# Optimization experiments

Measured on AMD Instinct MI355X. Metric: run time of the kernel, lower is better.

## Reference

```python
import jax, jax.numpy as jnp
import numpy as np

H = 356  # CHAR_EMBED_DIM (100) + ELMO_EMBED_DIM (256)
CHAR_VOCAB = 96
CHAR_DIM = 100
N_FILT = 100
KW = 5
N_CTX = 8192
N_Q = 1024
W_CHARS = 16


def setup_inputs() -> dict:
    key = jax.random.key(0)
    ks = iter(jax.random.split(key, 32))
    s = 0.05
    inp = {}
    inp['ctx_char_ids'] = jax.random.randint(next(ks), (N_CTX, W_CHARS), 0, CHAR_VOCAB, dtype=jnp.int32)
    inp['q_char_ids'] = jax.random.randint(next(ks), (N_Q, W_CHARS), 0, CHAR_VOCAB, dtype=jnp.int32)
    inp['ctx_elmo'] = jax.random.normal(next(ks), (N_CTX, 256), jnp.float32)
    inp['q_elmo'] = jax.random.normal(next(ks), (N_Q, 256), jnp.float32)
    inp['char_emb'] = jax.random.normal(next(ks), (CHAR_VOCAB, CHAR_DIM), jnp.float32)
    inp['conv_w'] = jax.random.normal(next(ks), (N_FILT, CHAR_DIM, KW), jnp.float32) * s
    inp['conv_b'] = jax.random.normal(next(ks), (N_FILT,), jnp.float32) * s
    # Highway: 2 layers of plain + gate Linear(356 -> 356)
    inp['hw_pw'] = jax.random.normal(next(ks), (2, H, H), jnp.float32) * s
    inp['hw_pb'] = jax.random.normal(next(ks), (2, H), jnp.float32) * s
    inp['hw_gw'] = jax.random.normal(next(ks), (2, H, H), jnp.float32) * s
    inp['hw_gb'] = jax.random.normal(next(ks), (2, H), jnp.float32) * s
    # BiLSTM layer 0: input 356; layer 1: input 712. dims: [dir, 4H, Din]
    inp['w_ih0'] = jax.random.normal(next(ks), (2, 4 * H, H), jnp.float32) * s
    inp['w_hh0'] = jax.random.normal(next(ks), (2, 4 * H, H), jnp.float32) * s
    inp['b_ih0'] = jax.random.normal(next(ks), (2, 4 * H), jnp.float32) * s
    inp['b_hh0'] = jax.random.normal(next(ks), (2, 4 * H), jnp.float32) * s
    inp['w_ih1'] = jax.random.normal(next(ks), (2, 4 * H, 2 * H), jnp.float32) * s
    inp['w_hh1'] = jax.random.normal(next(ks), (2, 4 * H, H), jnp.float32) * s
    inp['b_ih1'] = jax.random.normal(next(ks), (2, 4 * H), jnp.float32) * s
    inp['b_hh1'] = jax.random.normal(next(ks), (2, 4 * H), jnp.float32) * s
    # randomize_init_hidden=True: random (h0, c0), shared per original code.
    h0 = jax.random.normal(next(ks), (2, 2, H), jnp.float32)  # [layer, dir, H]
    inp['h0'] = h0
    inp['c0'] = h0  # original returns (init_hidden, init_hidden)
    return inp


def _highway(x, pw, pb, gw, gb):
    for i in range(2):
        g = jax.nn.sigmoid(x @ gw[i].T + gb[i])
        p = jax.nn.relu(x @ pw[i].T + pb[i])
        x = g * p + (1.0 - g) * x
    return x


def _lstm_dir(x, w_ih, w_hh, b_ih, b_hh, h0, c0):
    # x: [T, Din]; PyTorch gate order i, f, g, o
    xg = x @ w_ih.T + (b_ih + b_hh)  # [T, 4H]

    def step(carry, xg_t):
        h, c = carry
        gates = xg_t + h @ w_hh.T
        i, f, g, o = jnp.split(gates, 4)
        i = jax.nn.sigmoid(i)
        f = jax.nn.sigmoid(f)
        g = jnp.tanh(g)
        o = jax.nn.sigmoid(o)
        c = f * c + i * g
        h = o * jnp.tanh(c)
        return (h, c), h

    _, hs = jax.lax.scan(step, (h0, c0), xg)
    return hs  # [T, H]


def _bilstm_layer(x, w_ih, w_hh, b_ih, b_hh, h0, c0):
    fwd = _lstm_dir(x, w_ih[0], w_hh[0], b_ih[0], b_hh[0], h0[0], c0[0])
    bwd = _lstm_dir(x[::-1], w_ih[1], w_hh[1], b_ih[1], b_hh[1], h0[1], c0[1])[::-1]
    return jnp.concatenate([fwd, bwd], axis=-1)  # [T, 2H]


def _embed_doc(char_ids, elmo, char_emb, conv_w, conv_b, hw_pw, hw_pb, hw_gw, hw_gb,
               w_ih0, w_hh0, b_ih0, b_hh0, w_ih1, w_hh1, b_ih1, b_hh1, h0, c0):
    ce = char_emb[char_ids]                  # [N, W, 100]
    x = jnp.transpose(ce, (0, 2, 1))         # [N, 100, W]
    conv = jax.lax.conv_general_dilated(
        x, conv_w, window_strides=(1,), padding=[(KW // 2, KW // 2)],
        dimension_numbers=('NCH', 'OIH', 'NCH')) + conv_b[None, :, None]
    cnn_feat = conv.max(axis=2)              # [N, 100] maxpool over char positions
    feats = jnp.concatenate([cnn_feat, elmo], axis=1)  # [N, 356]
    hwy = _highway(feats, hw_pw, hw_pb, hw_gw, hw_gb)
    l1 = _bilstm_layer(hwy, w_ih0, w_hh0, b_ih0, b_hh0, h0[0], c0[0])
    l2 = _bilstm_layer(l1, w_ih1, w_hh1, b_ih1, b_hh1, h0[1], c0[1])
    return l2  # [N, 712]


def reference(ctx_char_ids, q_char_ids, ctx_elmo, q_elmo, char_emb, conv_w, conv_b,
              hw_pw, hw_pb, hw_gw, hw_gb,
              w_ih0, w_hh0, b_ih0, b_hh0, w_ih1, w_hh1, b_ih1, b_hh1, h0, c0):
    params = (char_emb, conv_w, conv_b, hw_pw, hw_pb, hw_gw, hw_gb,
              w_ih0, w_hh0, b_ih0, b_hh0, w_ih1, w_hh1, b_ih1, b_hh1, h0, c0)
    ctx_out = _embed_doc(ctx_char_ids, ctx_elmo, *params)
    q_out = _embed_doc(q_char_ids, q_elmo, *params)
    return (ctx_out, q_out)
```

## Files before the change

kernel.cpp:

```cpp
#include <hip/hip_runtime.h>
#include <hip/hip_bf16.h>

#define H_DIM 356
#define G4 1424
#define NCTX 8192
#define NQ 1024
#define NTOT 9216
#define CDIM 100
#define NFILT 100
#define KW 5
#define WCH 16

typedef _Float16 f16_t;

__device__ __forceinline__ float sigmoidf_fast(float x) {
    return 1.0f / (1.0f + __expf(-x));
}
__device__ __forceinline__ float tanhf_fast(float x) {
    return 2.0f / (1.0f + __expf(-2.0f * x)) - 1.0f;
}
__device__ __forceinline__ unsigned pack_f16x2(float a, float b) {
    _Float16 ha = (_Float16)a, hb = (_Float16)b;
    unsigned short ua = __builtin_bit_cast(unsigned short, ha);
    unsigned short ub = __builtin_bit_cast(unsigned short, hb);
    return (unsigned)ua | ((unsigned)ub << 16);
}
__device__ __forceinline__ unsigned short f16_bits(float a) {
    _Float16 ha = (_Float16)a;
    return __builtin_bit_cast(unsigned short, ha);
}

#define FDOT_S(ACC, W, HS) \
    asm("v_dot2_f32_f16 %0, %1, %2, %0" : "+v"(ACC) : "v"(W), "s"(HS))

__global__ __launch_bounds__(128) void cnn_highway_kernel(
    const int* __restrict__ ctx_ids, const int* __restrict__ q_ids,
    const float* __restrict__ ctx_elmo, const float* __restrict__ q_elmo,
    const float* __restrict__ char_emb, const float* __restrict__ conv_w,
    const float* __restrict__ conv_b,
    const float* __restrict__ hw_pw, const float* __restrict__ hw_pb,
    const float* __restrict__ hw_gw, const float* __restrict__ hw_gb,
    float* __restrict__ feats_out)
{
    __shared__ float s_ce[WCH][CDIM];
    __shared__ float s_feats[16][H_DIM];
    const int tid  = threadIdx.x;
    const int row0 = blockIdx.x * 16;

    for (int rr = 0; rr < 16; ++rr) {
        const int row = row0 + rr;
        const int* ids = (row < NCTX) ? (ctx_ids + (size_t)row * WCH)
                                      : (q_ids + (size_t)(row - NCTX) * WCH);
        for (int idx = tid; idx < WCH * CDIM; idx += 128) {
            int w = idx / CDIM, c = idx - w * CDIM;
            s_ce[w][c] = char_emb[(size_t)ids[w] * CDIM + c];
        }
        __syncthreads();
        if (tid < NFILT) {
            const int f = tid;
            float s[WCH];
            float bias = conv_b[f];
            #pragma unroll
            for (int p = 0; p < WCH; ++p) s[p] = bias;
            const float* wrow = conv_w + (size_t)f * CDIM * KW;
            for (int c0 = 0; c0 < CDIM; c0 += 4) {
                float wv[20];
                const float4* wp4 = (const float4*)(wrow + c0 * KW);
                #pragma unroll
                for (int u = 0; u < 5; ++u) {
                    float4 v = wp4[u];
                    wv[u * 4 + 0] = v.x; wv[u * 4 + 1] = v.y;
                    wv[u * 4 + 2] = v.z; wv[u * 4 + 3] = v.w;
                }
                #pragma unroll
                for (int cc = 0; cc < 4; ++cc) {
                    float ce[WCH];
                    #pragma unroll
                    for (int w = 0; w < WCH; ++w) ce[w] = s_ce[w][c0 + cc];
                    #pragma unroll
                    for (int p = 0; p < WCH; ++p) {
                        #pragma unroll
                        for (int k = 0; k < KW; ++k) {
                            const int wpos = p + k - 2;
                            if (wpos >= 0 && wpos < WCH)
                                s[p] = fmaf(ce[wpos], wv[cc * 5 + k], s[p]);
                        }
                    }
                }
            }
            float m = s[0];
            #pragma unroll
            for (int p = 1; p < WCH; ++p) m = fmaxf(m, s[p]);
            s_feats[rr][f] = m;
        }
        __syncthreads();
    }

    for (int idx = tid; idx < 16 * 256; idx += 128) {
        int rr = idx >> 8, c = idx & 255;
        int row = row0 + rr;
        float v = (row < NCTX) ? ctx_elmo[(size_t)row * 256 + c]
                               : q_elmo[(size_t)(row - NCTX) * 256 + c];
        s_feats[rr][CDIM + c] = v;
    }
    __syncthreads();

    for (int l = 0; l < 2; ++l) {
        float newv[3][16];
        for (int it = 0; it < 3; ++it) {
            const int j = it * 128 + tid;
            if (j < H_DIM) {
                float accP[16], accG[16];
                #pragma unroll
                for (int r = 0; r < 16; ++r) { accP[r] = 0.0f; accG[r] = 0.0f; }
                const float* pw = hw_pw + ((size_t)l * H_DIM + j) * H_DIM;
                const float* gw = hw_gw + ((size_t)l * H_DIM + j) * H_DIM;
                for (int k0 = 0; k0 < H_DIM; k0 += 4) {
                    float4 wpv4 = *(const float4*)(pw + k0);
                    float4 wgv4 = *(const float4*)(gw + k0);
                    float wp[4] = {wpv4.x, wpv4.y, wpv4.z, wpv4.w};
                    float wg[4] = {wgv4.x, wgv4.y, wgv4.z, wgv4.w};
                    #pragma unroll
                    for (int kk = 0; kk < 4; ++kk) {
                        #pragma unroll
                        for (int r = 0; r < 16; ++r) {
                            float fv = s_feats[r][k0 + kk];
                            accP[r] = fmaf(fv, wp[kk], accP[r]);
                            accG[r] = fmaf(fv, wg[kk], accG[r]);
                        }
                    }
                }
                const float pb = hw_pb[l * H_DIM + j];
                const float gb = hw_gb[l * H_DIM + j];
                #pragma unroll
                for (int r = 0; r < 16; ++r) {
                    float p = accP[r] + pb; p = p > 0.0f ? p : 0.0f;
                    float g = sigmoidf_fast(accG[r] + gb);
                    newv[it][r] = g * p + (1.0f - g) * s_feats[r][j];
                }
            }
        }
        __syncthreads();
        for (int it = 0; it < 3; ++it) {
            const int j = it * 128 + tid;
            if (j < H_DIM) {
                #pragma unroll
                for (int r = 0; r < 16; ++r) s_feats[r][j] = newv[it][r];
            }
        }
        __syncthreads();
    }

    for (int idx = tid; idx < 16 * H_DIM; idx += 128) {
        int rr = idx / H_DIM, j = idx - rr * H_DIM;
        feats_out[(size_t)(row0 + rr) * H_DIM + j] = s_feats[rr][j];
    }
}

__global__ __launch_bounds__(256) void gemm_nt_bias_kernel(
    const float* __restrict__ A, const float* __restrict__ B,
    const float* __restrict__ bia, const float* __restrict__ bib,
    f16_t* __restrict__ C, int M, int N, int K)
{
    const int z = blockIdx.z;
    const float* Bz = B + (size_t)z * N * K;
    f16_t* Cz = C + (size_t)z * M * N;
    const int n0 = blockIdx.x * 64;
    const int m0 = blockIdx.y * 64;
    __shared__ float As[64][17];
    __shared__ float Bs[64][17];
    const int tid = threadIdx.x;
    const int tx = tid & 15, ty = tid >> 4;
    const int lr = tid >> 2;
    const int lc = (tid & 3) * 4;
    float acc[4][4];
    #pragma unroll
    for (int i = 0; i < 4; ++i)
        #pragma unroll
        for (int j = 0; j < 4; ++j) acc[i][j] = 0.0f;

    const int ktiles = (K + 15) / 16;
    for (int kt = 0; kt < ktiles; ++kt) {
        const int k0 = kt * 16;
        float4 av = {0, 0, 0, 0}, bv = {0, 0, 0, 0};
        if (k0 + lc < K)
            av = *(const float4*)(A + (size_t)(m0 + lr) * K + k0 + lc);
        const int bn = n0 + lr;
        if (bn < N && k0 + lc < K)
            bv = *(const float4*)(Bz + (size_t)bn * K + k0 + lc);
        __syncthreads();
        As[lr][lc + 0] = av.x; As[lr][lc + 1] = av.y;
        As[lr][lc + 2] = av.z; As[lr][lc + 3] = av.w;
        Bs[lr][lc + 0] = bv.x; Bs[lr][lc + 1] = bv.y;
        Bs[lr][lc + 2] = bv.z; Bs[lr][lc + 3] = bv.w;
        __syncthreads();
        #pragma unroll
        for (int kk = 0; kk < 16; ++kk) {
            float a[4], b[4];
            #pragma unroll
            for (int i = 0; i < 4; ++i) a[i] = As[ty * 4 + i][kk];
            #pragma unroll
            for (int j = 0; j < 4; ++j) b[j] = Bs[tx * 4 + j][kk];
            #pragma unroll
            for (int i = 0; i < 4; ++i)
                #pragma unroll
                for (int j = 0; j < 4; ++j)
                    acc[i][j] = fmaf(a[i], b[j], acc[i][j]);
        }
    }
    #pragma unroll
    for (int j = 0; j < 4; ++j) {
        const int n = n0 + tx * 4 + j;
        if (n < N) {
            const float bsum = bia[(size_t)z * N + n] + bib[(size_t)z * N + n];
            #pragma unroll
            for (int i = 0; i < 4; ++i) {
                const int m = m0 + ty * 4 + i;
                Cz[(size_t)m * N + n] = (f16_t)(acc[i][j] + bsum);
            }
        }
    }
}

__global__ __launch_bounds__(768)
__attribute__((amdgpu_waves_per_eu(3, 3)))
void lstm_scan8_kernel(
    const f16_t* __restrict__ xg,
    const float* __restrict__ whh,
    const float* __restrict__ h0,
    const float* __restrict__ c0,
    float* __restrict__ out,
    unsigned* hbuf,
    int tagbase)
{
    const int bid = blockIdx.x;
    const int s = bid & 7;
    if (s >= 4) return;
    const int sub = bid >> 3;
    const int doc = s >> 1, dir = s & 1;
    const int T = doc ? NQ : NCTX;
    const int rbase = doc ? NCTX : 0;
    const int soff = (s == 0) ? 0 : (s == 1) ? 8193 : (s == 2) ? 16386 : 17411;
    unsigned* hb = hbuf + (size_t)soff * 384;
    const int cnt = (sub < 4) ? 45 : 44;
    const int os  = 44 * sub + (sub < 4 ? sub : 4);
    const int tid = threadIdx.x;
    const int lane = tid & 63;

    __shared__ float s_part[4][192];

    const int wvi = tid >> 6;
    const int qd  = wvi & 3;
    const int rgp = wvi >> 2;
    const int r   = rgp * 64 + lane;
    const bool act = (r < 4 * cnt);
    const int gate = act ? (r / cnt) : 0;
    const int off  = act ? (r - gate * cnt) : 0;
    const int grow = gate * H_DIM + os + off;

    unsigned w[48];
    if (act) {
        const float* wrow = whh + ((size_t)dir * G4 + grow) * H_DIM + 89 * qd;
        #pragma unroll
        for (int p = 0; p < 44; ++p)
            w[p] = pack_f16x2(wrow[2 * p], wrow[2 * p + 1]);
        w[44] = pack_f16x2(wrow[88], 0.0f);
        w[45] = 0u; w[46] = 0u; w[47] = 0u;
    } else {
        #pragma unroll
        for (int p = 0; p < 48; ++p) w[p] = 0u;
    }

    const int npub = cnt + (sub < 4 ? 7 : 0);
    int pubw = 0;
    if (tid < npub) {
        if (tid < cnt) {
            const int i = os + tid;
            pubw = 96 * (i / 89) + (i % 89);
        } else {
            pubw = 96 * sub + 89 + (tid - cnt);
        }
    }

    float c_state = 0.0f;
    if (tid < npub) {
        unsigned short hv = 0;
        if (tid < cnt) {
            c_state = c0[dir * H_DIM + os + tid];
            hv = f16_bits(h0[dir * H_DIM + os + tid]);
        }
        __hip_atomic_store(&hb[pubw], ((unsigned)(tagbase + 1) << 16) | hv,
                           __ATOMIC_RELAXED, __HIP_MEMORY_SCOPE_AGENT);
    }

    const f16_t* xgd = xg + (size_t)dir * NTOT * G4;

    for (int t = 0; t < T; ++t) {
        const int row = rbase + (dir ? (T - 1 - t) : t);
        float xv = 0.0f;
        if (qd == 0 && act) xv = (float)xgd[(size_t)row * G4 + grow];

        const unsigned want = (unsigned)(tagbase + t + 1);
        const unsigned* hw_ = hb + (size_t)t * 384 + 96 * qd;
        const int kb = (lane < 24) ? 4 * lane : 92;
        unsigned w0, w1, w2, w3;
        do {
            w0 = __hip_atomic_load(&hw_[kb],     __ATOMIC_RELAXED,
                                   __HIP_MEMORY_SCOPE_AGENT);
            w1 = __hip_atomic_load(&hw_[kb + 1], __ATOMIC_RELAXED,
                                   __HIP_MEMORY_SCOPE_AGENT);
            w2 = __hip_atomic_load(&hw_[kb + 2], __ATOMIC_RELAXED,
                                   __HIP_MEMORY_SCOPE_AGENT);
            w3 = __hip_atomic_load(&hw_[kb + 3], __ATOMIC_RELAXED,
                                   __HIP_MEMORY_SCOPE_AGENT);
        } while ((w0 >> 16) != want || (w1 >> 16) != want ||
                 (w2 >> 16) != want || (w3 >> 16) != want);
        const unsigned p0 = (w0 & 0xffffu) | (w1 << 16);
        const unsigned p1 = (w2 & 0xffffu) | (w3 << 16);

        float a0 = xv, a1 = 0.0f, a2 = 0.0f, a3 = 0.0f;
        #pragma unroll
        for (int q = 0; q < 48; q += 4) {
            const unsigned h0q = __builtin_amdgcn_readlane(p0, (q >> 1));
            const unsigned h1q = __builtin_amdgcn_readlane(p1, (q >> 1));
            const unsigned h2q = __builtin_amdgcn_readlane(p0, (q >> 1) + 1);
            const unsigned h3q = __builtin_amdgcn_readlane(p1, (q >> 1) + 1);
            FDOT_S(a0, w[q],     h0q);
            FDOT_S(a1, w[q + 1], h1q);
            FDOT_S(a2, w[q + 2], h2q);
            FDOT_S(a3, w[q + 3], h3q);
        }
        if (act) s_part[qd][r] = (a0 + a1) + (a2 + a3);
        __syncthreads();

        if (tid < npub) {
            unsigned short hvbits = 0;
            if (tid < cnt) {
                const float gi = s_part[0][tid] + s_part[1][tid]
                               + s_part[2][tid] + s_part[3][tid];
                const float gf = s_part[0][cnt + tid] + s_part[1][cnt + tid]
                               + s_part[2][cnt + tid] + s_part[3][cnt + tid];
                const float gg = s_part[0][2*cnt + tid] + s_part[1][2*cnt + tid]
                               + s_part[2][2*cnt + tid] + s_part[3][2*cnt + tid];
                const float go = s_part[0][3*cnt + tid] + s_part[1][3*cnt + tid]
                               + s_part[2][3*cnt + tid] + s_part[3][3*cnt + tid];
                const float ii = sigmoidf_fast(gi);
                const float ff = sigmoidf_fast(gf);
                const float gt = tanhf_fast(gg);
                const float oo = sigmoidf_fast(go);
                c_state = ff * c_state + ii * gt;
                const float hh = oo * tanhf_fast(c_state);
                out[(size_t)row * 712 + dir * H_DIM + os + tid] = hh;
                hvbits = f16_bits(hh);
            }
            __hip_atomic_store(&hb[(size_t)(t + 1) * 384 + pubw],
                               ((unsigned)(tagbase + t + 2) << 16) | hvbits,
                               __ATOMIC_RELAXED, __HIP_MEMORY_SCOPE_AGENT);
        }
        __syncthreads();
    }
}

extern "C" void kernel_launch(void* const* d_in, const int* in_sizes, int n_in,
                              void* d_out, int out_size, void* d_ws, size_t ws_size,
                              hipStream_t stream) {
    (void)in_sizes; (void)n_in; (void)out_size; (void)ws_size;
    const int*   ctx_ids  = (const int*)d_in[0];
    const int*   q_ids    = (const int*)d_in[1];
    const float* ctx_elmo = (const float*)d_in[2];
    const float* q_elmo   = (const float*)d_in[3];
    const float* char_emb = (const float*)d_in[4];
    const float* conv_w   = (const float*)d_in[5];
    const float* conv_b   = (const float*)d_in[6];
    const float* hw_pw    = (const float*)d_in[7];
    const float* hw_pb    = (const float*)d_in[8];
    const float* hw_gw    = (const float*)d_in[9];
    const float* hw_gb    = (const float*)d_in[10];
    const float* w_ih0    = (const float*)d_in[11];
    const float* w_hh0    = (const float*)d_in[12];
    const float* b_ih0    = (const float*)d_in[13];
    const float* b_hh0    = (const float*)d_in[14];
    const float* w_ih1    = (const float*)d_in[15];
    const float* w_hh1    = (const float*)d_in[16];
    const float* b_ih1    = (const float*)d_in[17];
    const float* b_hh1    = (const float*)d_in[18];
    const float* h0       = (const float*)d_in[19];
    const float* c0       = (const float*)d_in[20];
    float* out = (float*)d_out;

    f16_t* xg    = (f16_t*)d_ws;
    float* feats = (float*)((char*)d_ws + (size_t)2 * NTOT * G4 * sizeof(f16_t));
    float* l1out = feats + (size_t)NTOT * H_DIM;
    unsigned* hbuf = (unsigned*)(l1out + (size_t)NTOT * 712);

    hipMemsetAsync(hbuf, 0, (size_t)18436 * 384 * sizeof(unsigned), stream);

    cnn_highway_kernel<<<NTOT / 16, 128, 0, stream>>>(
        ctx_ids, q_ids, ctx_elmo, q_elmo, char_emb, conv_w, conv_b,
        hw_pw, hw_pb, hw_gw, hw_gb, feats);

    dim3 ggrid((G4 + 63) / 64, NTOT / 64, 2);
    gemm_nt_bias_kernel<<<ggrid, 256, 0, stream>>>(
        feats, w_ih0, b_ih0, b_hh0, xg, NTOT, G4, H_DIM);

    lstm_scan8_kernel<<<64, 768, 0, stream>>>(
        xg, w_hh0, h0, c0, l1out, hbuf, 0);

    gemm_nt_bias_kernel<<<ggrid, 256, 0, stream>>>(
        l1out, w_ih1, b_ih1, b_hh1, xg, NTOT, G4, 2 * H_DIM);

    lstm_scan8_kernel<<<64, 768, 0, stream>>>(
        xg, w_hh1, h0 + 2 * H_DIM, c0 + 2 * H_DIM, out, hbuf, 16384);
}
```

Baseline: 32.42 ms.

## Double-buffer LSTM partial sums, drop second barrier, prefetch next handoff line

Double-buffers the shared partial-sum array by step parity so the second __syncthreads per recurrent step can be removed. The handoff slot for step t+2 is touched early with an atomic fetch-add of zero, meant to warm that cache line before the spin-wait reaches it. The h store to the output array is moved after the publish, so the next step's hidden state becomes visible sooner. This cuts per-step latency on the serial recurrence, but the atomic RMW on lines other blocks write could add contention, and the single barrier depends on the parity buffers for correctness.

```diff
diff --git a/kernel.cpp b/kernel.cpp
--- a/kernel.cpp
+++ b/kernel.cpp
@@ -247,7 +247,7 @@
     const int tid = threadIdx.x;
     const int lane = tid & 63;
 
-    __shared__ float s_part[4][192];
+    __shared__ float s_part[2][4][192];
 
     const int wvi = tid >> 6;
     const int qd  = wvi & 3;
@@ -294,15 +294,22 @@
     }
 
     const f16_t* xgd = xg + (size_t)dir * NTOT * G4;
+    const bool pf_lane = (wvi < 4) && (lane < 24) && ((lane & 7) == 0);
+    const int kb = (lane < 24) ? 4 * lane : 92;
 
     for (int t = 0; t < T; ++t) {
         const int row = rbase + (dir ? (T - 1 - t) : t);
         float xv = 0.0f;
         if (qd == 0 && act) xv = (float)xgd[(size_t)row * G4 + grow];
 
+        if (pf_lane && (t + 2 <= T)) {
+            unsigned* pf = hb + (size_t)(t + 2) * 384 + 96 * qd + kb;
+            __hip_atomic_fetch_add(pf, 0u, __ATOMIC_RELAXED,
+                                   __HIP_MEMORY_SCOPE_AGENT);
+        }
+
         const unsigned want = (unsigned)(tagbase + t + 1);
         const unsigned* hw_ = hb + (size_t)t * 384 + 96 * qd;
-        const int kb = (lane < 24) ? 4 * lane : 92;
         unsigned w0, w1, w2, w3;
         do {
             w0 = __hip_atomic_load(&hw_[kb],     __ATOMIC_RELAXED,
@@ -330,34 +337,36 @@
             FDOT_S(a2, w[q + 2], h2q);
             FDOT_S(a3, w[q + 3], h3q);
         }
-        if (act) s_part[qd][r] = (a0 + a1) + (a2 + a3);
+        float (*sp)[192] = s_part[t & 1];
+        if (act) sp[qd][r] = (a0 + a1) + (a2 + a3);
         __syncthreads();
 
         if (tid < npub) {
             unsigned short hvbits = 0;
+            float hh = 0.0f;
             if (tid < cnt) {
-                const float gi = s_part[0][tid] + s_part[1][tid]
-                               + s_part[2][tid] + s_part[3][tid];
-                const float gf = s_part[0][cnt + tid] + s_part[1][cnt + tid]
-                               + s_part[2][cnt + tid] + s_part[3][cnt + tid];
-                const float gg = s_part[0][2*cnt + tid] + s_part[1][2*cnt + tid]
-                               + s_part[2][2*cnt + tid] + s_part[3][2*cnt + tid];
-                const float go = s_part[0][3*cnt + tid] + s_part[1][3*cnt + tid]
-                               + s_part[2][3*cnt + tid] + s_part[3][3*cnt + tid];
+                const float gi = sp[0][tid] + sp[1][tid]
+                               + sp[2][tid] + sp[3][tid];
+                const float gf = sp[0][cnt + tid] + sp[1][cnt + tid]
+                               + sp[2][cnt + tid] + sp[3][cnt + tid];
+                const float gg = sp[0][2*cnt + tid] + sp[1][2*cnt + tid]
+                               + sp[2][2*cnt + tid] + sp[3][2*cnt + tid];
+                const float go = sp[0][3*cnt + tid] + sp[1][3*cnt + tid]
+                               + sp[2][3*cnt + tid] + sp[3][3*cnt + tid];
                 const float ii = sigmoidf_fast(gi);
                 const float ff = sigmoidf_fast(gf);
                 const float gt = tanhf_fast(gg);
                 const float oo = sigmoidf_fast(go);
                 c_state = ff * c_state + ii * gt;
-                const float hh = oo * tanhf_fast(c_state);
-                out[(size_t)row * 712 + dir * H_DIM + os + tid] = hh;
+                hh = oo * tanhf_fast(c_state);
                 hvbits = f16_bits(hh);
             }
             __hip_atomic_store(&hb[(size_t)(t + 1) * 384 + pubw],
                                ((unsigned)(tagbase + t + 2) << 16) | hvbits,
                                __ATOMIC_RELAXED, __HIP_MEMORY_SCOPE_AGENT);
-        }
-        __syncthreads();
+            if (tid < cnt)
+                out[(size_t)row * 712 + dir * H_DIM + os + tid] = hh;
+        }
     }
 }
 
```

Result: slower. 34.83 ms (+7.4%).

## Stage polled hidden state via LDS, prefetch next x-gate, reorder publish

Applied to the files above, without the earlier changes.

In the LSTM scan, only the first wave group polls the global hidden-state handoff buffer and stages the values in shared memory for the other wave group, which removes redundant global spin traffic. The next timestep's input-gate value is loaded early to hide its latency. The trailing barrier per step is dropped, and the cell update moves to wave 4 so the atomic publish happens before the output store. This shortens the per-step critical path of the serial recurrence, but adds an LDS round trip and a barrier after polling, and relies on the remaining barriers to keep s_stage and s_part reuse safe across steps.

```diff
diff --git a/kernel.cpp b/kernel.cpp
--- a/kernel.cpp
+++ b/kernel.cpp
@@ -248,6 +248,7 @@
     const int lane = tid & 63;
 
     __shared__ float s_part[4][192];
+    __shared__ __align__(16) unsigned s_stage[4][96];
 
     const int wvi = tid >> 6;
     const int qd  = wvi & 3;
@@ -273,52 +274,68 @@
 
     const int npub = cnt + (sub < 4 ? 7 : 0);
     int pubw = 0;
-    if (tid < npub) {
-        if (tid < cnt) {
-            const int i = os + tid;
+    if (wvi == 4 && lane < npub) {
+        if (lane < cnt) {
+            const int i = os + lane;
             pubw = 96 * (i / 89) + (i % 89);
         } else {
-            pubw = 96 * sub + 89 + (tid - cnt);
+            pubw = 96 * sub + 89 + (lane - cnt);
         }
     }
 
     float c_state = 0.0f;
-    if (tid < npub) {
+    if (wvi == 4 && lane < npub) {
         unsigned short hv = 0;
-        if (tid < cnt) {
-            c_state = c0[dir * H_DIM + os + tid];
-            hv = f16_bits(h0[dir * H_DIM + os + tid]);
+        if (lane < cnt) {
+            c_state = c0[dir * H_DIM + os + lane];
+            hv = f16_bits(h0[dir * H_DIM + os + lane]);
         }
         __hip_atomic_store(&hb[pubw], ((unsigned)(tagbase + 1) << 16) | hv,
                            __ATOMIC_RELAXED, __HIP_MEMORY_SCOPE_AGENT);
     }
 
     const f16_t* xgd = xg + (size_t)dir * NTOT * G4;
+    const int kb = (lane < 24) ? 4 * lane : 92;
+
+    float xv_cur = 0.0f;
+    if (qd == 0 && act) {
+        const int row0_ = rbase + (dir ? (T - 1) : 0);
+        xv_cur = (float)xgd[(size_t)row0_ * G4 + grow];
+    }
 
     for (int t = 0; t < T; ++t) {
         const int row = rbase + (dir ? (T - 1 - t) : t);
-        float xv = 0.0f;
-        if (qd == 0 && act) xv = (float)xgd[(size_t)row * G4 + grow];
-
         const unsigned want = (unsigned)(tagbase + t + 1);
-        const unsigned* hw_ = hb + (size_t)t * 384 + 96 * qd;
-        const int kb = (lane < 24) ? 4 * lane : 92;
+
         unsigned w0, w1, w2, w3;
-        do {
-            w0 = __hip_atomic_load(&hw_[kb],     __ATOMIC_RELAXED,
-                                   __HIP_MEMORY_SCOPE_AGENT);
-            w1 = __hip_atomic_load(&hw_[kb + 1], __ATOMIC_RELAXED,
-                                   __HIP_MEMORY_SCOPE_AGENT);
-            w2 = __hip_atomic_load(&hw_[kb + 2], __ATOMIC_RELAXED,
-                                   __HIP_MEMORY_SCOPE_AGENT);
-            w3 = __hip_atomic_load(&hw_[kb + 3], __ATOMIC_RELAXED,
-                                   __HIP_MEMORY_SCOPE_AGENT);
-        } while ((w0 >> 16) != want || (w1 >> 16) != want ||
-                 (w2 >> 16) != want || (w3 >> 16) != want);
+        if (rgp == 0) {
+            const unsigned* hw_ = hb + (size_t)t * 384 + 96 * qd;
+            do {
+                w0 = __hip_atomic_load(&hw_[kb],     __ATOMIC_RELAXED,
+                                       __HIP_MEMORY_SCOPE_AGENT);
+                w1 = __hip_atomic_load(&hw_[kb + 1], __ATOMIC_RELAXED,
+                                       __HIP_MEMORY_SCOPE_AGENT);
+                w2 = __hip_atomic_load(&hw_[kb + 2], __ATOMIC_RELAXED,
+                                       __HIP_MEMORY_SCOPE_AGENT);
+                w3 = __hip_atomic_load(&hw_[kb + 3], __ATOMIC_RELAXED,
+                                       __HIP_MEMORY_SCOPE_AGENT);
+            } while ((w0 >> 16) != want || (w1 >> 16) != want ||
+                     (w2 >> 16) != want || (w3 >> 16) != want);
+            if (lane < 24) {
+                s_stage[qd][kb + 0] = w0; s_stage[qd][kb + 1] = w1;
+                s_stage[qd][kb + 2] = w2; s_stage[qd][kb + 3] = w3;
+            }
+        }
+        __syncthreads();
+
+        if (rgp != 0) {
+            w0 = s_stage[qd][kb];     w1 = s_stage[qd][kb + 1];
+            w2 = s_stage[qd][kb + 2]; w3 = s_stage[qd][kb + 3];
+        }
         const unsigned p0 = (w0 & 0xffffu) | (w1 << 16);
         const unsigned p1 = (w2 & 0xffffu) | (w3 << 16);
 
-        float a0 = xv, a1 = 0.0f, a2 = 0.0f, a3 = 0.0f;
+        float a0 = xv_cur, a1 = 0.0f, a2 = 0.0f, a3 = 0.0f;
         #pragma unroll
         for (int q = 0; q < 48; q += 4) {
             const unsigned h0q = __builtin_amdgcn_readlane(p0, (q >> 1));
@@ -333,31 +350,39 @@
         if (act) s_part[qd][r] = (a0 + a1) + (a2 + a3);
         __syncthreads();
 
-        if (tid < npub) {
+        float xv_next = 0.0f;
+        if (t + 1 < T && qd == 0 && act) {
+            const int row_next = rbase + (dir ? (T - 2 - t) : (t + 1));
+            xv_next = (float)xgd[(size_t)row_next * G4 + grow];
+        }
+
+        if (wvi == 4 && lane < npub) {
             unsigned short hvbits = 0;
-            if (tid < cnt) {
-                const float gi = s_part[0][tid] + s_part[1][tid]
-                               + s_part[2][tid] + s_part[3][tid];
-                const float gf = s_part[0][cnt + tid] + s_part[1][cnt + tid]
-                               + s_part[2][cnt + tid] + s_part[3][cnt + tid];
-                const float gg = s_part[0][2*cnt + tid] + s_part[1][2*cnt + tid]
-                               + s_part[2][2*cnt + tid] + s_part[3][2*cnt + tid];
-                const float go = s_part[0][3*cnt + tid] + s_part[1][3*cnt + tid]
-                               + s_part[2][3*cnt + tid] + s_part[3][3*cnt + tid];
+            float hh = 0.0f;
+            if (lane < cnt) {
+                const float gi = s_part[0][lane] + s_part[1][lane]
+                               + s_part[2][lane] + s_part[3][lane];
+                const float gf = s_part[0][cnt + lane] + s_part[1][cnt + lane]
+                               + s_part[2][cnt + lane] + s_part[3][cnt + lane];
+                const float gg = s_part[0][2*cnt + lane] + s_part[1][2*cnt + lane]
+                               + s_part[2][2*cnt + lane] + s_part[3][2*cnt + lane];
+                const float go = s_part[0][3*cnt + lane] + s_part[1][3*cnt + lane]
+                               + s_part[2][3*cnt + lane] + s_part[3][3*cnt + lane];
                 const float ii = sigmoidf_fast(gi);
                 const float ff = sigmoidf_fast(gf);
                 const float gt = tanhf_fast(gg);
                 const float oo = sigmoidf_fast(go);
                 c_state = ff * c_state + ii * gt;
-                const float hh = oo * tanhf_fast(c_state);
-                out[(size_t)row * 712 + dir * H_DIM + os + tid] = hh;
+                hh = oo * tanhf_fast(c_state);
                 hvbits = f16_bits(hh);
             }
             __hip_atomic_store(&hb[(size_t)(t + 1) * 384 + pubw],
                                ((unsigned)(tagbase + t + 2) << 16) | hvbits,
                                __ATOMIC_RELAXED, __HIP_MEMORY_SCOPE_AGENT);
-        }
-        __syncthreads();
+            if (lane < cnt)
+                out[(size_t)row * 712 + dir * H_DIM + os + lane] = hh;
+        }
+        xv_cur = xv_next;
     }
 }
 
@@ -393,7 +418,8 @@
     float* l1out = feats + (size_t)NTOT * H_DIM;
     unsigned* hbuf = (unsigned*)(l1out + (size_t)NTOT * 712);
 
-    hipMemsetAsync(hbuf, 0, (size_t)18436 * 384 * sizeof(unsigned), stream);
+    (void)hipMemsetAsync(hbuf, 0, (size_t)18436 * 384 * sizeof(unsigned),
+                         stream);
 
     cnn_highway_kernel<<<NTOT / 16, 128, 0, stream>>>(
         ctx_ids, q_ids, ctx_elmo, q_elmo, char_emb, conv_w, conv_b,
```

Measured after the change: 33.46 ms. +3.2%, slower.
